# Performance work log

Hardware: AMD Instinct MI355X
Metric: run time of the kernel (lower is better)

The kernel has to match this reference:

```python
import jax, jax.numpy as jnp
import numpy as np

G = 8          # grid_size
NUM_HEADS = 8


def setup_inputs() -> dict:
    key = jax.random.key(0)
    ks = jax.random.split(key, 4)
    B, H, W, C = 32, 64, 64, 256
    x = jax.random.normal(ks[0], (B, H, W, C), dtype=jnp.float32)
    w_qkv = jax.random.normal(ks[1], (3 * C, C), dtype=jnp.float32) * (C ** -0.5)
    b_qkv = jnp.zeros((3 * C,), dtype=jnp.float32)
    w_proj = jax.random.normal(ks[2], (C, C), dtype=jnp.float32) * (C ** -0.5)
    b_proj = jnp.zeros((C,), dtype=jnp.float32)
    return {"x": x, "w_qkv": w_qkv, "b_qkv": b_qkv, "w_proj": w_proj, "b_proj": b_proj}


def reference(x, w_qkv, b_qkv, w_proj, b_proj):
    B, H, W, C = x.shape
    g = G
    nh = NUM_HEADS
    hd = C // nh
    scale = hd ** -0.5
    Hp, Wp = H // g, W // g
    # grid partition: [B,H,W,C] -> [B*Hp*Wp, g*g, C]
    t = x.reshape(B, g, Hp, g, Wp, C)
    t = t.transpose(0, 2, 4, 1, 3, 5).reshape(B * Hp * Wp, g * g, C)
    Bg, N = t.shape[0], g * g
    # qkv projection (torch Linear: x @ W.T + b)
    qkv = t @ w_qkv.T + b_qkv                       # [Bg, N, 3C]
    qkv = qkv.reshape(Bg, N, 3, nh, hd).transpose(2, 0, 3, 1, 4)  # [3, Bg, nh, N, hd]
    q, k, v = qkv[0], qkv[1], qkv[2]
    attn = jnp.einsum('bhnd,bhmd->bhnm', q, k) * scale
    attn = jax.nn.softmax(attn, axis=-1)
    out = jnp.einsum('bhnm,bhmd->bhnd', attn, v)    # [Bg, nh, N, hd]
    out = out.transpose(0, 2, 1, 3).reshape(Bg, N, C)
    out = out @ w_proj.T + b_proj
    # grid unpartition: [Bg, g, g, C] -> [B, H, W, C]
    out = out.reshape(B, Hp, Wp, g, g, C).transpose(0, 3, 1, 4, 2, 5).reshape(B, H, W, C)
    return out
```

## Files before the change

### kernel.cpp

```cpp
#include <hip/hip_runtime.h>

typedef __attribute__((ext_vector_type(8))) short bf16x8;
typedef __attribute__((ext_vector_type(4))) float f32x4;
typedef __attribute__((ext_vector_type(4))) short s16x4;

#define MFMA16(a, b, c) __builtin_amdgcn_mfma_f32_16x16x32_bf16((a), (b), (c), 0, 0, 0)

__device__ __forceinline__ short f2bf(float f) {
    union { float f; unsigned u; } v; v.f = f;
    return (short)((v.u + 0x7FFFu + ((v.u >> 16) & 1u)) >> 16);
}
__device__ __forceinline__ s16x4 cvt4(f32x4 v) {
    s16x4 r; r[0] = f2bf(v[0]); r[1] = f2bf(v[1]); r[2] = f2bf(v[2]); r[3] = f2bf(v[3]); return r;
}
__device__ __forceinline__ f32x4 fzero4() { f32x4 z; z[0]=0.f; z[1]=0.f; z[2]=0.f; z[3]=0.f; return z; }

__global__ __launch_bounds__(256, 1)
void convw_kernel(const float* __restrict__ wqkv, const float* __restrict__ wproj,
                  short* __restrict__ wsb)
{
    int i = (blockIdx.x * 256 + threadIdx.x) * 8;
    const float* src = (i < 196608) ? (wqkv + i) : (wproj + (i - 196608));
    *(s16x4*)(wsb + i)     = cvt4(*(const f32x4*)(src));
    *(s16x4*)(wsb + i + 4) = cvt4(*(const f32x4*)(src + 4));
}

#define SMEM_BYTES 70656

__global__ __launch_bounds__(256, 2)
void ga2d_kernel(const float* __restrict__ x,
                 const short* __restrict__ wsb,
                 const float* __restrict__ bqkv,
                 const float* __restrict__ bproj,
                 float* __restrict__ out)
{
    extern __shared__ short smem[];
    short* XA = smem;
    const int tid  = threadIdx.x;
    const int w    = tid >> 6;
    const int lane = tid & 63;
    const int l16  = lane & 15;
    const int q4   = lane >> 4;
    short* SW = smem + 16896 + w * 4608;

    const int blk = blockIdx.x;
    const int bb  = blk >> 6;
    const int hp  = (blk >> 3) & 7;
    const int wp  = blk & 7;
    const size_t gbase = (size_t)bb * 64 * 64 * 256;

    #pragma unroll
    for (int i = 0; i < 16; ++i) {
        int id  = i * 256 + tid;
        int tok = id >> 6, c4 = id & 63;
        int hr  = (tok >> 3) * 8 + hp;
        int wc  = (tok & 7) * 8 + wp;
        f32x4 v = *(const f32x4*)(x + gbase + ((size_t)hr * 64 + wc) * 256 + c4 * 4);
        *(s16x4*)(XA + tok * 264 + c4 * 4) = cvt4(v);
    }
    __syncthreads();

    bf16x8 qa[2][4], kb[2][4], vb[2][2][2];
    #pragma unroll
    for (int g3 = 0; g3 < 3; ++g3) {
        const short* WB = wsb + (size_t)(g3 * 256 + w * 64) * 256;
        f32x4 acc[4][4];
        #pragma unroll
        for (int n = 0; n < 4; ++n)
            #pragma unroll
            for (int m = 0; m < 4; ++m) acc[n][m] = fzero4();
        #pragma unroll
        for (int k = 0; k < 8; ++k) {
            const int koff = k * 32 + q4 * 8;
            bf16x8 a[4], bw[4];
            #pragma unroll
            for (int m = 0; m < 4; ++m)
                a[m] = *(const bf16x8*)(XA + (m * 16 + l16) * 264 + koff);
            #pragma unroll
            for (int n = 0; n < 4; ++n)
                bw[n] = *(const bf16x8*)(WB + (size_t)(n * 16 + l16) * 256 + koff);
            #pragma unroll
            for (int n = 0; n < 4; ++n)
                #pragma unroll
                for (int m = 0; m < 4; ++m)
                    acc[n][m] = MFMA16(a[m], bw[n], acc[n][m]);
        }
        if (g3 < 2) {
            #pragma unroll
            for (int n = 0; n < 4; ++n) {
                const float bi = bqkv[g3 * 256 + w * 64 + n * 16 + l16];
                #pragma unroll
                for (int m = 0; m < 4; ++m)
                    #pragma unroll
                    for (int r = 0; r < 4; ++r)
                        SW[(m * 16 + q4 * 4 + r) * 72 + n * 16 + l16] = f2bf(acc[n][m][r] + bi);
            }
        } else {
            #pragma unroll
            for (int n = 0; n < 4; ++n) {
                const float bi = bqkv[512 + w * 64 + n * 16 + l16];
                #pragma unroll
                for (int m = 0; m < 4; ++m) {
                    s16x4 pk;
                    #pragma unroll
                    for (int r = 0; r < 4; ++r) pk[r] = f2bf(acc[n][m][r] + bi);
                    *(s16x4*)(SW + (n * 16 + l16) * 72 + m * 16 + q4 * 4) = pk;
                }
            }
        }
        if (g3 == 0) {
            #pragma unroll
            for (int hl = 0; hl < 2; ++hl)
                #pragma unroll
                for (int m = 0; m < 4; ++m)
                    qa[hl][m] = *(const bf16x8*)(SW + (m * 16 + l16) * 72 + hl * 32 + q4 * 8);
        } else if (g3 == 1) {
            #pragma unroll
            for (int hl = 0; hl < 2; ++hl)
                #pragma unroll
                for (int n = 0; n < 4; ++n)
                    kb[hl][n] = *(const bf16x8*)(SW + (n * 16 + l16) * 72 + hl * 32 + q4 * 8);
        } else {
            #pragma unroll
            for (int hl = 0; hl < 2; ++hl)
                #pragma unroll
                for (int dt = 0; dt < 2; ++dt)
                    #pragma unroll
                    for (int kt = 0; kt < 2; ++kt)
                        vb[hl][dt][kt] = *(const bf16x8*)(SW + (hl * 32 + dt * 16 + l16) * 72 + kt * 32 + q4 * 8);
        }
    }
    __syncthreads();

    const float kscl = 0.25503546f;
    #pragma unroll
    for (int hl = 0; hl < 2; ++hl) {
        f32x4 s[4][4];
        #pragma unroll
        for (int m = 0; m < 4; ++m)
            #pragma unroll
            for (int n = 0; n < 4; ++n)
                s[m][n] = MFMA16(qa[hl][m], kb[hl][n], fzero4());

        float rinv[4][4];
        #pragma unroll
        for (int m = 0; m < 4; ++m) {
            #pragma unroll
            for (int r = 0; r < 4; ++r) {
                float v = fmaxf(fmaxf(s[m][0][r], s[m][1][r]), fmaxf(s[m][2][r], s[m][3][r]));
                v = fmaxf(v, __shfl_xor(v, 1));
                v = fmaxf(v, __shfl_xor(v, 2));
                v = fmaxf(v, __shfl_xor(v, 4));
                v = fmaxf(v, __shfl_xor(v, 8));
                float t = 0.f;
                #pragma unroll
                for (int n = 0; n < 4; ++n) {
                    s[m][n][r] = exp2f((s[m][n][r] - v) * kscl);
                    t += s[m][n][r];
                }
                t += __shfl_xor(t, 1);
                t += __shfl_xor(t, 2);
                t += __shfl_xor(t, 4);
                t += __shfl_xor(t, 8);
                rinv[m][r] = 1.0f / t;
            }
        }
        #pragma unroll
        for (int m = 0; m < 4; ++m)
            #pragma unroll
            for (int n = 0; n < 4; ++n)
                #pragma unroll
                for (int r = 0; r < 4; ++r)
                    SW[(m * 16 + q4 * 4 + r) * 72 + n * 16 + l16] = f2bf(s[m][n][r]);

        f32x4 o[4][2];
        #pragma unroll
        for (int m = 0; m < 4; ++m) { o[m][0] = fzero4(); o[m][1] = fzero4(); }
        #pragma unroll
        for (int kt = 0; kt < 2; ++kt) {
            bf16x8 pa[4];
            #pragma unroll
            for (int m = 0; m < 4; ++m)
                pa[m] = *(const bf16x8*)(SW + (m * 16 + l16) * 72 + kt * 32 + q4 * 8);
            #pragma unroll
            for (int m = 0; m < 4; ++m)
                #pragma unroll
                for (int dt = 0; dt < 2; ++dt)
                    o[m][dt] = MFMA16(pa[m], vb[hl][dt][kt], o[m][dt]);
        }
        #pragma unroll
        for (int m = 0; m < 4; ++m)
            #pragma unroll
            for (int dt = 0; dt < 2; ++dt)
                #pragma unroll
                for (int r = 0; r < 4; ++r)
                    XA[(m * 16 + q4 * 4 + r) * 264 + w * 64 + hl * 32 + dt * 16 + l16] =
                        f2bf(o[m][dt][r] * rinv[m][r]);
    }
    __syncthreads();

    {
        const short* WPb = wsb + 196608 + (size_t)(w * 64) * 256;
        f32x4 pc[4][4];
        #pragma unroll
        for (int n = 0; n < 4; ++n)
            #pragma unroll
            for (int m = 0; m < 4; ++m) pc[n][m] = fzero4();
        #pragma unroll
        for (int k = 0; k < 8; ++k) {
            const int koff = k * 32 + q4 * 8;
            bf16x8 a[4], bw[4];
            #pragma unroll
            for (int m = 0; m < 4; ++m)
                a[m] = *(const bf16x8*)(XA + (m * 16 + l16) * 264 + koff);
            #pragma unroll
            for (int n = 0; n < 4; ++n)
                bw[n] = *(const bf16x8*)(WPb + (size_t)(n * 16 + l16) * 256 + koff);
            #pragma unroll
            for (int n = 0; n < 4; ++n)
                #pragma unroll
                for (int m = 0; m < 4; ++m)
                    pc[n][m] = MFMA16(a[m], bw[n], pc[n][m]);
        }
        #pragma unroll
        for (int n = 0; n < 4; ++n) {
            const int col  = w * 64 + n * 16 + l16;
            const float bi = bproj[col];
            #pragma unroll
            for (int m = 0; m < 4; ++m) {
                #pragma unroll
                for (int r = 0; r < 4; ++r) {
                    const int tok = m * 16 + q4 * 4 + r;
                    const int hr  = (tok >> 3) * 8 + hp;
                    const int wc  = (tok & 7) * 8 + wp;
                    out[gbase + ((size_t)hr * 64 + wc) * 256 + col] = pc[n][m][r] + bi;
                }
            }
        }
    }
}

extern "C" void kernel_launch(void* const* d_in, const int* in_sizes, int n_in,
                              void* d_out, int out_size, void* d_ws, size_t ws_size,
                              hipStream_t stream) {
    const float* x     = (const float*)d_in[0];
    const float* wqkv  = (const float*)d_in[1];
    const float* bqkv  = (const float*)d_in[2];
    const float* wproj = (const float*)d_in[3];
    const float* bproj = (const float*)d_in[4];
    float*       out   = (float*)d_out;
    short*       wsb   = (short*)d_ws;

    convw_kernel<<<128, 256, 0, stream>>>(wqkv, wproj, wsb);

    hipFuncSetAttribute(reinterpret_cast<const void*>(ga2d_kernel),
                        hipFuncAttributeMaxDynamicSharedMemorySize, SMEM_BYTES);
    ga2d_kernel<<<2048, 256, SMEM_BYTES, stream>>>(x, wsb, bqkv, bproj, out);
}
```

Measured before the change: 375.3 us.

## Transpose MFMA operands for vectorized stores, shrink scratch LDS, raise occupancy

Swaps the A/B operands of the Q/K, score, PV and output-projection MFMAs so each lane holds contiguous output columns. Scratch LDS writes become packed 4-wide bf16 stores, the final global stores become float4 writes, and the softmax reductions use cross-quad shuffles. The per-wave scratch buffer is halved into two ping-pong 32-row halves, which cuts shared memory to 52 KB so launch bounds can target 3 blocks per CU. This adds more store/read rounds and raises register pressure under the tighter occupancy bound.

Result: slower. 383.7 us (+2.2%).

```diff
diff --git a/kernel.cpp b/kernel.cpp
--- a/kernel.cpp
+++ b/kernel.cpp
@@ -25,9 +25,68 @@
     *(s16x4*)(wsb + i + 4) = cvt4(*(const f32x4*)(src + 4));
 }
 
-#define SMEM_BYTES 70656
-
-__global__ __launch_bounds__(256, 2)
+#define SMEM_BYTES 52224
+
+
+#define QK_ST(HL, MH, B)  { \
+    _Pragma("unroll") \
+    for (int n2 = 0; n2 < 2; ++n2) { \
+      _Pragma("unroll") \
+      for (int m2 = 0; m2 < 2; ++m2) { \
+        s16x4 pk; \
+        _Pragma("unroll") \
+        for (int r = 0; r < 4; ++r) \
+          pk[r] = f2bf(acc[2*(HL)+n2][2*(MH)+m2][r] + bq[2*(HL)+n2][r]); \
+        *(s16x4*)((B) + (m2*16 + l16)*36 + n2*16 + q4*4) = pk; \
+      } \
+    } }
+
+#define QK_RD(HL, MH, B, DST)  { \
+    _Pragma("unroll") \
+    for (int m2 = 0; m2 < 2; ++m2) \
+      DST[HL][2*(MH)+m2] = *(const bf16x8*)((B) + (m2*16 + l16)*36 + q4*8); }
+
+#define QK_ROUNDS(DST) \
+    QK_ST(0,0,SW0) QK_ST(0,1,SW1) QK_RD(0,0,SW0,DST) QK_ST(1,0,SW0) \
+    QK_RD(0,1,SW1,DST) QK_ST(1,1,SW1) QK_RD(1,0,SW0,DST) QK_RD(1,1,SW1,DST)
+
+#define V_ST(HL, KT, B)  { \
+    _Pragma("unroll") \
+    for (int n2 = 0; n2 < 2; ++n2) { \
+      _Pragma("unroll") \
+      for (int m2 = 0; m2 < 2; ++m2) { \
+        s16x4 pk; \
+        _Pragma("unroll") \
+        for (int r = 0; r < 4; ++r) \
+          pk[r] = f2bf(acc[2*(HL)+n2][2*(KT)+m2][r] + bv[2*(HL)+n2]); \
+        *(s16x4*)((B) + (n2*16 + l16)*36 + m2*16 + q4*4) = pk; \
+      } \
+    } }
+
+#define V_RD(HL, KT, B)  { \
+    _Pragma("unroll") \
+    for (int dt = 0; dt < 2; ++dt) \
+      vb[HL][dt][KT] = *(const bf16x8*)((B) + (dt*16 + l16)*36 + q4*8); }
+
+#define P_ST(KT, MH, B)  { \
+    _Pragma("unroll") \
+    for (int n2 = 0; n2 < 2; ++n2) { \
+      _Pragma("unroll") \
+      for (int m2 = 0; m2 < 2; ++m2) { \
+        s16x4 pk; \
+        _Pragma("unroll") \
+        for (int r = 0; r < 4; ++r) \
+          pk[r] = f2bf(s[2*(KT)+n2][2*(MH)+m2][r]); \
+        *(s16x4*)((B) + (m2*16 + l16)*36 + n2*16 + q4*4) = pk; \
+      } \
+    } }
+
+#define P_RD(MH, B)  { \
+    _Pragma("unroll") \
+    for (int m2 = 0; m2 < 2; ++m2) \
+      pa[2*(MH)+m2] = *(const bf16x8*)((B) + (m2*16 + l16)*36 + q4*8); }
+
+__global__ __launch_bounds__(256, 3)
 void ga2d_kernel(const float* __restrict__ x,
                  const short* __restrict__ wsb,
                  const float* __restrict__ bqkv,
@@ -41,7 +100,8 @@
     const int lane = tid & 63;
     const int l16  = lane & 15;
     const int q4   = lane >> 4;
-    short* SW = smem + 16896 + w * 4608;
+    short* SW0 = smem + 16896 + w * 2304;
+    short* SW1 = SW0 + 1152;
 
     const int blk = blockIdx.x;
     const int bb  = blk >> 6;
@@ -79,55 +139,32 @@
             #pragma unroll
             for (int n = 0; n < 4; ++n)
                 bw[n] = *(const bf16x8*)(WB + (size_t)(n * 16 + l16) * 256 + koff);
-            #pragma unroll
-            for (int n = 0; n < 4; ++n)
-                #pragma unroll
-                for (int m = 0; m < 4; ++m)
-                    acc[n][m] = MFMA16(a[m], bw[n], acc[n][m]);
+            if (g3 < 2) {
+                #pragma unroll
+                for (int n = 0; n < 4; ++n)
+                    #pragma unroll
+                    for (int m = 0; m < 4; ++m)
+                        acc[n][m] = MFMA16(bw[n], a[m], acc[n][m]);
+            } else {
+                #pragma unroll
+                for (int n = 0; n < 4; ++n)
+                    #pragma unroll
+                    for (int m = 0; m < 4; ++m)
+                        acc[n][m] = MFMA16(a[m], bw[n], acc[n][m]);
+            }
         }
         if (g3 < 2) {
-            #pragma unroll
-            for (int n = 0; n < 4; ++n) {
-                const float bi = bqkv[g3 * 256 + w * 64 + n * 16 + l16];
-                #pragma unroll
-                for (int m = 0; m < 4; ++m)
-                    #pragma unroll
-                    for (int r = 0; r < 4; ++r)
-                        SW[(m * 16 + q4 * 4 + r) * 72 + n * 16 + l16] = f2bf(acc[n][m][r] + bi);
-            }
+            f32x4 bq[4];
+            #pragma unroll
+            for (int n = 0; n < 4; ++n)
+                bq[n] = *(const f32x4*)(bqkv + g3 * 256 + w * 64 + n * 16 + q4 * 4);
+            if (g3 == 0) { QK_ROUNDS(qa) } else { QK_ROUNDS(kb) }
         } else {
-            #pragma unroll
-            for (int n = 0; n < 4; ++n) {
-                const float bi = bqkv[512 + w * 64 + n * 16 + l16];
-                #pragma unroll
-                for (int m = 0; m < 4; ++m) {
-                    s16x4 pk;
-                    #pragma unroll
-                    for (int r = 0; r < 4; ++r) pk[r] = f2bf(acc[n][m][r] + bi);
-                    *(s16x4*)(SW + (n * 16 + l16) * 72 + m * 16 + q4 * 4) = pk;
-                }
-            }
-        }
-        if (g3 == 0) {
-            #pragma unroll
-            for (int hl = 0; hl < 2; ++hl)
-                #pragma unroll
-                for (int m = 0; m < 4; ++m)
-                    qa[hl][m] = *(const bf16x8*)(SW + (m * 16 + l16) * 72 + hl * 32 + q4 * 8);
-        } else if (g3 == 1) {
-            #pragma unroll
-            for (int hl = 0; hl < 2; ++hl)
-                #pragma unroll
-                for (int n = 0; n < 4; ++n)
-                    kb[hl][n] = *(const bf16x8*)(SW + (n * 16 + l16) * 72 + hl * 32 + q4 * 8);
-        } else {
-            #pragma unroll
-            for (int hl = 0; hl < 2; ++hl)
-                #pragma unroll
-                for (int dt = 0; dt < 2; ++dt)
-                    #pragma unroll
-                    for (int kt = 0; kt < 2; ++kt)
-                        vb[hl][dt][kt] = *(const bf16x8*)(SW + (hl * 32 + dt * 16 + l16) * 72 + kt * 32 + q4 * 8);
+            float bv[4];
+            #pragma unroll
+            for (int n = 0; n < 4; ++n) bv[n] = bqkv[512 + w * 64 + n * 16 + l16];
+            V_ST(0,0,SW0) V_ST(0,1,SW1) V_RD(0,0,SW0) V_ST(1,0,SW0)
+            V_RD(0,1,SW1) V_ST(1,1,SW1) V_RD(1,0,SW0) V_RD(1,1,SW1)
         }
     }
     __syncthreads();
@@ -137,65 +174,59 @@
     for (int hl = 0; hl < 2; ++hl) {
         f32x4 s[4][4];
         #pragma unroll
-        for (int m = 0; m < 4; ++m)
-            #pragma unroll
-            for (int n = 0; n < 4; ++n)
-                s[m][n] = MFMA16(qa[hl][m], kb[hl][n], fzero4());
-
-        float rinv[4][4];
+        for (int n = 0; n < 4; ++n)
+            #pragma unroll
+            for (int m = 0; m < 4; ++m)
+                s[n][m] = MFMA16(kb[hl][n], qa[hl][m], fzero4());
+
+        float rinv[4];
         #pragma unroll
         for (int m = 0; m < 4; ++m) {
-            #pragma unroll
-            for (int r = 0; r < 4; ++r) {
-                float v = fmaxf(fmaxf(s[m][0][r], s[m][1][r]), fmaxf(s[m][2][r], s[m][3][r]));
-                v = fmaxf(v, __shfl_xor(v, 1));
-                v = fmaxf(v, __shfl_xor(v, 2));
-                v = fmaxf(v, __shfl_xor(v, 4));
-                v = fmaxf(v, __shfl_xor(v, 8));
-                float t = 0.f;
-                #pragma unroll
-                for (int n = 0; n < 4; ++n) {
-                    s[m][n][r] = exp2f((s[m][n][r] - v) * kscl);
-                    t += s[m][n][r];
+            float v0 = fmaxf(fmaxf(s[0][m][0], s[0][m][1]), fmaxf(s[0][m][2], s[0][m][3]));
+            float v1 = fmaxf(fmaxf(s[1][m][0], s[1][m][1]), fmaxf(s[1][m][2], s[1][m][3]));
+            float v2 = fmaxf(fmaxf(s[2][m][0], s[2][m][1]), fmaxf(s[2][m][2], s[2][m][3]));
+            float v3 = fmaxf(fmaxf(s[3][m][0], s[3][m][1]), fmaxf(s[3][m][2], s[3][m][3]));
+            float v  = fmaxf(fmaxf(v0, v1), fmaxf(v2, v3));
+            v = fmaxf(v, __shfl_xor(v, 16));
+            v = fmaxf(v, __shfl_xor(v, 32));
+            float t = 0.f;
+            #pragma unroll
+            for (int n = 0; n < 4; ++n)
+                #pragma unroll
+                for (int r = 0; r < 4; ++r) {
+                    float e = exp2f((s[n][m][r] - v) * kscl);
+                    s[n][m][r] = e;
+                    t += e;
                 }
-                t += __shfl_xor(t, 1);
-                t += __shfl_xor(t, 2);
-                t += __shfl_xor(t, 4);
-                t += __shfl_xor(t, 8);
-                rinv[m][r] = 1.0f / t;
-            }
-        }
-        #pragma unroll
-        for (int m = 0; m < 4; ++m)
-            #pragma unroll
-            for (int n = 0; n < 4; ++n)
-                #pragma unroll
-                for (int r = 0; r < 4; ++r)
-                    SW[(m * 16 + q4 * 4 + r) * 72 + n * 16 + l16] = f2bf(s[m][n][r]);
-
-        f32x4 o[4][2];
-        #pragma unroll
-        for (int m = 0; m < 4; ++m) { o[m][0] = fzero4(); o[m][1] = fzero4(); }
+            t += __shfl_xor(t, 16);
+            t += __shfl_xor(t, 32);
+            rinv[m] = 1.0f / t;
+        }
+
+        f32x4 o2[2][4];
+        #pragma unroll
+        for (int dt = 0; dt < 2; ++dt)
+            #pragma unroll
+            for (int m = 0; m < 4; ++m) o2[dt][m] = fzero4();
         #pragma unroll
         for (int kt = 0; kt < 2; ++kt) {
             bf16x8 pa[4];
-            #pragma unroll
-            for (int m = 0; m < 4; ++m)
-                pa[m] = *(const bf16x8*)(SW + (m * 16 + l16) * 72 + kt * 32 + q4 * 8);
+            P_ST(kt,0,SW0) P_ST(kt,1,SW1) P_RD(0,SW0) P_RD(1,SW1)
             #pragma unroll
             for (int m = 0; m < 4; ++m)
                 #pragma unroll
                 for (int dt = 0; dt < 2; ++dt)
-                    o[m][dt] = MFMA16(pa[m], vb[hl][dt][kt], o[m][dt]);
-        }
-        #pragma unroll
-        for (int m = 0; m < 4; ++m)
-            #pragma unroll
-            for (int dt = 0; dt < 2; ++dt)
-                #pragma unroll
-                for (int r = 0; r < 4; ++r)
-                    XA[(m * 16 + q4 * 4 + r) * 264 + w * 64 + hl * 32 + dt * 16 + l16] =
-                        f2bf(o[m][dt][r] * rinv[m][r]);
+                    o2[dt][m] = MFMA16(vb[hl][dt][kt], pa[m], o2[dt][m]);
+        }
+        #pragma unroll
+        for (int dt = 0; dt < 2; ++dt)
+            #pragma unroll
+            for (int m = 0; m < 4; ++m) {
+                s16x4 pk;
+                #pragma unroll
+                for (int r = 0; r < 4; ++r) pk[r] = f2bf(o2[dt][m][r] * rinv[m]);
+                *(s16x4*)(XA + (m * 16 + l16) * 264 + w * 64 + hl * 32 + dt * 16 + q4 * 4) = pk;
+            }
     }
     __syncthreads();
 
@@ -220,21 +251,20 @@
             for (int n = 0; n < 4; ++n)
                 #pragma unroll
                 for (int m = 0; m < 4; ++m)
-                    pc[n][m] = MFMA16(a[m], bw[n], pc[n][m]);
+                    pc[n][m] = MFMA16(bw[n], a[m], pc[n][m]);
         }
         #pragma unroll
         for (int n = 0; n < 4; ++n) {
-            const int col  = w * 64 + n * 16 + l16;
-            const float bi = bproj[col];
+            const f32x4 bp = *(const f32x4*)(bproj + w * 64 + n * 16 + q4 * 4);
             #pragma unroll
             for (int m = 0; m < 4; ++m) {
-                #pragma unroll
-                for (int r = 0; r < 4; ++r) {
-                    const int tok = m * 16 + q4 * 4 + r;
-                    const int hr  = (tok >> 3) * 8 + hp;
-                    const int wc  = (tok & 7) * 8 + wp;
-                    out[gbase + ((size_t)hr * 64 + wc) * 256 + col] = pc[n][m][r] + bi;
-                }
+                const int tok = m * 16 + l16;
+                const int hr  = (tok >> 3) * 8 + hp;
+                const int wc  = (tok & 7) * 8 + wp;
+                f32x4 rv;
+                #pragma unroll
+                for (int r = 0; r < 4; ++r) rv[r] = pc[n][m][r] + bp[r];
+                *(f32x4*)(out + gbase + ((size_t)hr * 64 + wc) * 256 + w * 64 + n * 16 + q4 * 4) = rv;
             }
         }
     }
```
